# Optimization experiments

Hardware: AMD Instinct MI355X
Metric: run time of the kernel (lower is better)

Reference implementation:

```python
import jax, jax.numpy as jnp
import numpy as np

NEG = -1e30  # finite stand-in for log(0); safe for logaddexp and its gradient


def setup_inputs() -> dict:
    key = jax.random.key(0)
    k1, k2 = jax.random.split(key)
    B, T, C, U = 256, 512, 128, 128
    logits = jax.random.normal(k1, (B, T, C), dtype=jnp.float32)
    y_pred = jax.nn.softmax(logits, axis=-1)  # ctc_batch_cost expects probabilities
    y_true = jax.random.randint(k2, (B, U), 0, C - 1)  # labels exclude blank=C-1
    return {"y_true": y_true, "y_pred": y_pred}


def _ctc_batch_cost(y_true, y_pred):
    """Keras-style CTC: blank = num_classes-1, logp = log(y_pred + 1e-7),
    full input_length = T and label_length = U for every row (as in the layer).
    Returns loss of shape [B, 1]."""
    B, T, C = y_pred.shape
    U = y_true.shape[1]
    blank = C - 1
    S = 2 * U + 1  # extended label: blank-interleaved
    logp = jnp.log(y_pred + 1e-7)  # [B,T,C], keras epsilon

    # extended label sequence z = [blank, l1, blank, l2, ..., lU, blank]
    ext = jnp.full((B, S), blank, dtype=y_true.dtype).at[:, 1::2].set(y_true)

    # lp[t,b,s] = logp[b,t,ext[b,s]]
    lp = jnp.take_along_axis(logp, jnp.broadcast_to(ext[:, None, :], (B, T, S)), axis=2)
    lp = jnp.transpose(lp, (1, 0, 2))  # [T,B,S]

    # skip transition s-2 -> s allowed iff z[s] != blank and z[s] != z[s-2]
    ext_m2 = jnp.pad(ext, ((0, 0), (2, 0)), constant_values=blank)[:, :S]
    skip = (ext != blank) & (ext != ext_m2)
    skip = skip.at[:, :2].set(False)  # no s-2 predecessor for s in {0,1}

    alpha0 = jnp.full((B, S), NEG, dtype=logp.dtype)
    alpha0 = alpha0.at[:, 0].set(lp[0, :, 0]).at[:, 1].set(lp[0, :, 1])

    def step(a, lp_t):
        a1 = jnp.pad(a, ((0, 0), (1, 0)), constant_values=NEG)[:, :S]
        a2 = jnp.pad(a, ((0, 0), (2, 0)), constant_values=NEG)[:, :S]
        a2 = jnp.where(skip, a2, NEG)
        a = jnp.logaddexp(jnp.logaddexp(a, a1), a2) + lp_t
        return a, None

    aT, _ = jax.lax.scan(step, alpha0, lp[1:])
    loss = -jnp.logaddexp(aT[:, S - 1], aT[:, S - 2])
    return loss[:, None]  # [B,1], matching ctc_batch_cost output shape


def reference(y_true, y_pred):
    # The layer returns y_pred and registers the loss via add_loss; the loss is
    # the actual computation of interest, so we return it.
    return _ctc_batch_cost(y_true, y_pred)
```

## Files before the change

### kernel.cpp

```cpp
#include <hip/hip_runtime.h>

#define EPSF 1e-7f

#define DPPF0(x, ctrl) \
    __int_as_float(__builtin_amdgcn_update_dpp(0, __float_as_int(x), ctrl, 0xF, 0xF, false))

__device__ __forceinline__ float f_rcp(float x) { return __builtin_amdgcn_rcpf(x); }
__device__ __forceinline__ float wave_shr1_f(float x) { return DPPF0(x, 0x138); }

__device__ __forceinline__ float wave_max64(float x) {
    x = fmaxf(x, DPPF0(x, 0x111));
    x = fmaxf(x, DPPF0(x, 0x112));
    x = fmaxf(x, DPPF0(x, 0x114));
    x = fmaxf(x, DPPF0(x, 0x118));
    x = fmaxf(x, DPPF0(x, 0x142));
    x = fmaxf(x, DPPF0(x, 0x143));
    return __int_as_float(__builtin_amdgcn_readlane(__float_as_int(x), 63));
}

#define SB0() __builtin_amdgcn_sched_barrier(0)
#define WAITV(N) do { asm volatile("s_waitcnt vmcnt(" #N ")" ::: "memory"); SB0(); } while (0)

#define ISS(dst, voff, IMM) \
    asm volatile("global_load_dword %0, %1, %2 offset:" #IMM \
                 : "=v"(dst) : "v"(voff), "s"(pn))

#define GISSUE(X) do { \
    ISS(X##b[0], vb, 0);    ISS(X##1[0], v1, 0);    ISS(X##3[0], v3, 0); \
    ISS(X##b[1], vb, 512);  ISS(X##1[1], v1, 512);  ISS(X##3[1], v3, 512); \
    ISS(X##b[2], vb, 1024); ISS(X##1[2], v1, 1024); ISS(X##3[2], v3, 1024); \
    ISS(X##b[3], vb, 1536); ISS(X##1[3], v1, 1536); ISS(X##3[3], v3, 1536); \
    ISS(X##b[4], vb, 2048); ISS(X##1[4], v1, 2048); ISS(X##3[4], v3, 2048); \
    ISS(X##b[5], vb, 2560); ISS(X##1[5], v1, 2560); ISS(X##3[5], v3, 2560); \
    ISS(X##b[6], vb, 3072); ISS(X##1[6], v1, 3072); ISS(X##3[6], v3, 3072); \
    ISS(X##b[7], vb, 3584); ISS(X##1[7], v1, 3584); ISS(X##3[7], v3, 3584); \
    pn += 8 * 128; \
} while (0)

#define GISSUE_T7(X) do { \
    ISS(X##b[0], vb, 0);    ISS(X##1[0], v1, 0);    ISS(X##3[0], v3, 0); \
    ISS(X##b[1], vb, 512);  ISS(X##1[1], v1, 512);  ISS(X##3[1], v3, 512); \
    ISS(X##b[2], vb, 1024); ISS(X##1[2], v1, 1024); ISS(X##3[2], v3, 1024); \
    ISS(X##b[3], vb, 1536); ISS(X##1[3], v1, 1536); ISS(X##3[3], v3, 1536); \
    ISS(X##b[4], vb, 2048); ISS(X##1[4], v1, 2048); ISS(X##3[4], v3, 2048); \
    ISS(X##b[5], vb, 2560); ISS(X##1[5], v1, 2560); ISS(X##3[5], v3, 2560); \
    ISS(X##b[6], vb, 3072); ISS(X##1[6], v1, 3072); ISS(X##3[6], v3, 3072); \
} while (0)

#define PSTEP(PBE_, P1_, P3_) do { \
    const float e1 = (P1_) + EPSF; \
    const float e3 = (P3_) + EPSF; \
    const float n3 = wave_shr1_f(u3); \
    const float t1 = fmaf(m1, n3, u0 + u1); \
    const float t3 = fmaf(m3, u1, u2 + u3); \
    u4 = (u4 + u3) * (PBE_); \
    u3 = t3 * e3; \
    u2 = (u2 + u1) * (PBE_); \
    u1 = t1 * e1; \
    u0 = (u0 + n3) * (PBE_); \
} while (0)

#define SNAP(RM, LM) do { \
    float mm_ = fmaxf(fmaxf(u0, u1), fmaxf(u2, fmaxf(u3, u4))); \
    mm_ = wave_max64(mm_); \
    RM = f_rcp(mm_); \
    LM = __logf(mm_); \
} while (0)

#define APPLY(RM, LM) do { \
    u0 *= RM; u1 *= RM; u2 *= RM; u3 *= RM; u4 *= RM; \
    O += LM; \
} while (0)

#define PBE(X, k) const float pbe##k = X##b[k] + EPSF;

#define CONS8(X) do { \
    PBE(X,0) PBE(X,1) PBE(X,2) PBE(X,3) PBE(X,4) PBE(X,5) PBE(X,6) PBE(X,7) \
    PSTEP(pbe0, X##1[0], X##3[0]); \
    PSTEP(pbe1, X##1[1], X##3[1]); \
    APPLY(rmA, lmA); \
    PSTEP(pbe2, X##1[2], X##3[2]); \
    PSTEP(pbe3, X##1[3], X##3[3]); \
    SNAP(rmB, lmB); \
    PSTEP(pbe4, X##1[4], X##3[4]); \
    PSTEP(pbe5, X##1[5], X##3[5]); \
    APPLY(rmB, lmB); \
    PSTEP(pbe6, X##1[6], X##3[6]); \
    PSTEP(pbe7, X##1[7], X##3[7]); \
    SNAP(rmA, lmA); \
} while (0)

#define CONS_T7(X) do { \
    PBE(X,0) PBE(X,1) PBE(X,2) PBE(X,3) PBE(X,4) PBE(X,5) PBE(X,6) \
    PSTEP(pbe0, X##1[0], X##3[0]); \
    PSTEP(pbe1, X##1[1], X##3[1]); \
    APPLY(rmA, lmA); \
    PSTEP(pbe2, X##1[2], X##3[2]); \
    PSTEP(pbe3, X##1[3], X##3[3]); \
    SNAP(rmB, lmB); \
    PSTEP(pbe4, X##1[4], X##3[4]); \
    PSTEP(pbe5, X##1[5], X##3[5]); \
    APPLY(rmB, lmB); \
    PSTEP(pbe6, X##1[6], X##3[6]); \
} while (0)

__global__ __launch_bounds__(64, 1) void ctc_prod512(
        const int* __restrict__ y_true, const float* __restrict__ y_pred,
        float* __restrict__ out) {
    const int b    = blockIdx.x;
    const int lane = threadIdx.x;
    const float* __restrict__ yp = y_pred + (size_t)b * (512 * 128);

    const int2 lc = ((const int2*)(y_true + (size_t)b * 128))[lane];
    const int c1 = lc.x, c3 = lc.y;
    const int cp = __builtin_amdgcn_update_dpp(0, c3, 0x138, 0xF, 0xF, false);
    const float m1 = (lane > 0 && c1 != cp) ? 1.f : 0.f;
    const float m3 = (c3 != c1) ? 1.f : 0.f;

    float u0, u1, u2 = 0.f, u3 = 0.f, u4 = 0.f;
    {
        const float pvb = yp[127];
        const float pv1 = yp[c1];
        u0 = (lane == 0) ? pvb + EPSF : 0.f;
        u1 = (lane == 0) ? pv1 + EPSF : 0.f;
    }
    float O = 0.f;
    float rmA = 1.0f, lmA = 0.0f, rmB = 1.0f, lmB = 0.0f;

    const int vb = 127 * 4;
    const int v1 = c1 * 4;
    const int v3 = c3 * 4;
    const float* pn = yp + 128;

    WAITV(0);

    float Ab[8], A1[8], A3[8];
    float Bb[8], B1[8], B3[8];
    float Cb[8], C1[8], C3[8];

    GISSUE(A);
    GISSUE(B);

    for (int j = 0; j < 20; ++j) {
        WAITV(24); GISSUE(C); CONS8(A);
        WAITV(24); GISSUE(A); CONS8(B);
        WAITV(24); GISSUE(B); CONS8(C);
    }
    WAITV(24); GISSUE(C);    CONS8(A);
    WAITV(24); GISSUE_T7(A); CONS8(B);
    WAITV(21); CONS8(C);
    WAITV(0);  CONS_T7(A);

    if (lane == 63) out[b] = -(O + __logf(u3 + u4));
}

__global__ __launch_bounds__(64, 1) void ctc_scan_generic(
        const int* __restrict__ y_true, const float* __restrict__ y_pred,
        float* __restrict__ out, int T, int C, int U) {
    const int b    = blockIdx.x;
    const int lane = threadIdx.x;
    const int blank = C - 1;
    const float* __restrict__ yp = y_pred + (size_t)b * T * C;

    const int2 lc = ((const int2*)(y_true + (size_t)b * U))[lane];
    const int c1 = lc.x, c3 = lc.y;
    const int cp = __builtin_amdgcn_update_dpp(0, c3, 0x138, 0xF, 0xF, false);
    const float m1 = (lane > 0 && c1 != cp) ? 1.f : 0.f;
    const float m3 = (c3 != c1) ? 1.f : 0.f;

    float u0, u1, u2 = 0.f, u3 = 0.f, u4 = 0.f;
    u0 = (lane == 0) ? yp[blank] + EPSF : 0.f;
    u1 = (lane == 0) ? yp[c1] + EPSF : 0.f;
    float O = 0.f;
    float rmA = 1.0f, lmA = 0.0f;
    int kren = 0;

    for (int t = 1; t < T; ++t) {
        const float* row = yp + (size_t)t * C;
        const float pbe = row[blank] + EPSF;
        PSTEP(pbe, row[c1], row[c3]);
        if (++kren == 4) { SNAP(rmA, lmA); APPLY(rmA, lmA); kren = 0; }
    }
    if (lane == 63) out[b] = -(O + __logf(u3 + u4));
}

extern "C" void kernel_launch(void* const* d_in, const int* in_sizes, int n_in,
                              void* d_out, int out_size, void* d_ws, size_t ws_size,
                              hipStream_t stream) {
    const int*   y_true = (const int*)d_in[0];
    const float* y_pred = (const float*)d_in[1];
    float*       out    = (float*)d_out;

    const int B = out_size;
    const int U = in_sizes[0] / B;
    const int C = 128;
    const int T = in_sizes[1] / (B * C);

    if (T == 512 && C == 128 && U == 128) {
        ctc_prod512<<<B, 64, 0, stream>>>(y_true, y_pred, out);
    } else {
        ctc_scan_generic<<<B, 64, 0, stream>>>(y_true, y_pred, out, T, C, U);
    }
}
```

Measured before the change: 41.22 us.

## Split CTC into parallel pack pass and two-row bf16 ratio scan

Adds a pre-pass kernel that stages each batch row's probabilities through shared memory and writes label/blank probability ratios packed as two bf16 values per lane, plus the raw blank probabilities. The blank factor is pulled out of the recursion algebraically and its logs are summed in parallel up front. The scan kernel then runs two batch rows per wave, which gives more independent work to hide the serial dependency chain, and reads half as many words per step. The cost is an extra launch and a workspace round-trip, and bf16 rounding of the ratios may cost accuracy.

```diff
diff --git a/kernel.cpp b/kernel.cpp
--- a/kernel.cpp
+++ b/kernel.cpp
@@ -1,6 +1,8 @@
 #include <hip/hip_runtime.h>
 
 #define EPSF 1e-7f
+
+typedef unsigned int u32;
 
 #define DPPF0(x, ctrl) \
     __int_as_float(__builtin_amdgcn_update_dpp(0, __float_as_int(x), ctrl, 0xF, 0xF, false))
@@ -18,13 +20,223 @@
     return __int_as_float(__builtin_amdgcn_readlane(__float_as_int(x), 63));
 }
 
+__device__ __forceinline__ float wave_sum64(float x) {
+    x += DPPF0(x, 0x111);
+    x += DPPF0(x, 0x112);
+    x += DPPF0(x, 0x114);
+    x += DPPF0(x, 0x118);
+    x += DPPF0(x, 0x142);
+    x += DPPF0(x, 0x143);
+    return __int_as_float(__builtin_amdgcn_readlane(__float_as_int(x), 63));
+}
+
+__device__ __forceinline__ u32 pack_bf2(float a, float b) {
+    u32 ua = __float_as_uint(a), ub = __float_as_uint(b);
+    ua += 0x7FFFu + ((ua >> 16) & 1u);
+    ub += 0x7FFFu + ((ub >> 16) & 1u);
+    return (ua >> 16) | (ub & 0xFFFF0000u);
+}
+
+__global__ __launch_bounds__(512, 1) void ctc_pack512c(
+        const int* __restrict__ y_true, const float* __restrict__ y_pred,
+        u32* __restrict__ pk, float* __restrict__ pbf) {
+    __shared__ float stage[2][32][128];
+
+    const int b    = blockIdx.x;
+    const int tid  = threadIdx.x;
+    const int w    = tid >> 6;
+    const int lane = tid & 63;
+    const float* __restrict__ yp = y_pred + (size_t)b * (512 * 128);
+
+    const int2 lc = ((const int2*)(y_true + (size_t)b * 128))[lane];
+    const int c1 = lc.x, c3 = lc.y;
+
+    u32*   __restrict__ pkb  = pk  + (size_t)b * (512 * 64);
+    float* __restrict__ pbfb = pbf + (size_t)b * 512;
+
+    float4 r0, r1;
+    {
+        const float* src = yp;
+        r0 = *(const float4*)(src + (size_t)(tid >> 5) * 128 + ((tid & 31) << 2));
+        const int f1 = tid + 512;
+        r1 = *(const float4*)(src + (size_t)(f1 >> 5) * 128 + ((f1 & 31) << 2));
+        *(float4*)(&stage[0][tid >> 5][(tid & 31) << 2]) = r0;
+        *(float4*)(&stage[0][f1 >> 5][(f1 & 31) << 2]) = r1;
+    }
+    __syncthreads();
+
+    for (int k = 0; k < 16; ++k) {
+        if (k < 15) {
+            const float* src = yp + (size_t)(k + 1) * 32 * 128;
+            r0 = *(const float4*)(src + (size_t)(tid >> 5) * 128 + ((tid & 31) << 2));
+            const int f1 = tid + 512;
+            r1 = *(const float4*)(src + (size_t)(f1 >> 5) * 128 + ((f1 & 31) << 2));
+        }
+        {
+            const int buf = k & 1;
+            const int tb  = k * 32 + w * 4;
+#pragma unroll
+            for (int rr = 0; rr < 4; ++rr) {
+                const int r = w * 4 + rr;
+                const float p1  = stage[buf][r][c1];
+                const float p3  = stage[buf][r][c3];
+                const float pb  = stage[buf][r][127];
+                const float rpb = f_rcp(pb + EPSF);
+                pkb[(size_t)(tb + rr) * 64 + lane] =
+                    pack_bf2((p1 + EPSF) * rpb, (p3 + EPSF) * rpb);
+                if (lane == 0) pbfb[tb + rr] = pb;
+            }
+        }
+        if (k < 15) {
+            const int nb = (k + 1) & 1;
+            *(float4*)(&stage[nb][tid >> 5][(tid & 31) << 2]) = r0;
+            const int f1 = tid + 512;
+            *(float4*)(&stage[nb][f1 >> 5][(f1 & 31) << 2]) = r1;
+        }
+        __syncthreads();
+    }
+}
+
+
+#define STEPQ2(WA_, WB_) do { \
+    const u32 wa_ = (WA_), wb_ = (WB_); \
+    const float q1a = __uint_as_float(wa_ << 16); \
+    const float q3a = __uint_as_float(wa_ & 0xFFFF0000u); \
+    const float q1b = __uint_as_float(wb_ << 16); \
+    const float q3b = __uint_as_float(wb_ & 0xFFFF0000u); \
+    const float n3a = wave_shr1_f(uA3); \
+    const float n3b = wave_shr1_f(uB3); \
+    const float t1a = fmaf(m1A, n3a, uA0 + uA1); \
+    const float t1b = fmaf(m1B, n3b, uB0 + uB1); \
+    const float t3a = fmaf(m3A, uA1, uA2 + uA3); \
+    const float t3b = fmaf(m3B, uB1, uB2 + uB3); \
+    uA4 += uA3; uB4 += uB3; \
+    uA2 += uA1; uB2 += uB1; \
+    uA3 = t3a * q3a; uB3 = t3b * q3b; \
+    uA1 = t1a * q1a; uB1 = t1b * q1b; \
+    uA0 += n3a; uB0 += n3b; \
+} while (0)
+
+#define SNAPA(RM, LM) do { \
+    float mm_ = fmaxf(fmaxf(uA0, uA1), fmaxf(uA2, fmaxf(uA3, uA4))); \
+    mm_ = wave_max64(mm_); RM = f_rcp(mm_); LM = __logf(mm_); } while (0)
+#define SNAPB(RM, LM) do { \
+    float mm_ = fmaxf(fmaxf(uB0, uB1), fmaxf(uB2, fmaxf(uB3, uB4))); \
+    mm_ = wave_max64(mm_); RM = f_rcp(mm_); LM = __logf(mm_); } while (0)
+#define APPLYA(RM, LM) do { uA0*=RM; uA1*=RM; uA2*=RM; uA3*=RM; uA4*=RM; OA += LM; } while (0)
+#define APPLYB(RM, LM) do { uB0*=RM; uB1*=RM; uB2*=RM; uB3*=RM; uB4*=RM; OB += LM; } while (0)
+
+#define LDW2G(X, BASE) do { \
+    X##a0 = pkA[(size_t)((BASE)+0)*64 + lane]; X##b0 = pkB[(size_t)((BASE)+0)*64 + lane]; \
+    X##a1 = pkA[(size_t)((BASE)+1)*64 + lane]; X##b1 = pkB[(size_t)((BASE)+1)*64 + lane]; \
+    X##a2 = pkA[(size_t)((BASE)+2)*64 + lane]; X##b2 = pkB[(size_t)((BASE)+2)*64 + lane]; \
+    X##a3 = pkA[(size_t)((BASE)+3)*64 + lane]; X##b3 = pkB[(size_t)((BASE)+3)*64 + lane]; \
+    X##a4 = pkA[(size_t)((BASE)+4)*64 + lane]; X##b4 = pkB[(size_t)((BASE)+4)*64 + lane]; \
+    X##a5 = pkA[(size_t)((BASE)+5)*64 + lane]; X##b5 = pkB[(size_t)((BASE)+5)*64 + lane]; \
+    X##a6 = pkA[(size_t)((BASE)+6)*64 + lane]; X##b6 = pkB[(size_t)((BASE)+6)*64 + lane]; \
+    X##a7 = pkA[(size_t)((BASE)+7)*64 + lane]; X##b7 = pkB[(size_t)((BASE)+7)*64 + lane]; \
+} while (0)
+
+#define CONS8_2(X) do { \
+    STEPQ2(X##a0, X##b0); STEPQ2(X##a1, X##b1); \
+    APPLYA(rm1A, lm1A); APPLYB(rm1B, lm1B); \
+    STEPQ2(X##a2, X##b2); STEPQ2(X##a3, X##b3); \
+    SNAPA(rm2A, lm2A); SNAPB(rm2B, lm2B); \
+    STEPQ2(X##a4, X##b4); STEPQ2(X##a5, X##b5); \
+    APPLYA(rm2A, lm2A); APPLYB(rm2B, lm2B); \
+    STEPQ2(X##a6, X##b6); STEPQ2(X##a7, X##b7); \
+    SNAPA(rm1A, lm1A); SNAPB(rm1B, lm1B); \
+} while (0)
+
+#define CONS0_2(X) do { \
+    STEPQ2(X##a1, X##b1); STEPQ2(X##a2, X##b2); \
+    APPLYA(rm1A, lm1A); APPLYB(rm1B, lm1B); \
+    STEPQ2(X##a3, X##b3); STEPQ2(X##a4, X##b4); \
+    SNAPA(rm2A, lm2A); SNAPB(rm2B, lm2B); \
+    STEPQ2(X##a5, X##b5); STEPQ2(X##a6, X##b6); \
+    APPLYA(rm2A, lm2A); APPLYB(rm2B, lm2B); \
+    STEPQ2(X##a7, X##b7); \
+    SNAPA(rm1A, lm1A); SNAPB(rm1B, lm1B); \
+} while (0)
+
+__global__ __launch_bounds__(64, 1) void ctc_scan2r512(
+        const int* __restrict__ y_true, const float* __restrict__ y_pred,
+        const u32* __restrict__ pk, const float* __restrict__ pbf,
+        float* __restrict__ out) {
+    const int blk  = blockIdx.x;
+    const int lane = threadIdx.x;
+    const int rA = 2 * blk, rB = 2 * blk + 1;
+    const float* __restrict__ ypA = y_pred + (size_t)rA * (512 * 128);
+    const float* __restrict__ ypB = y_pred + (size_t)rB * (512 * 128);
+    const u32* __restrict__ pkA = pk + (size_t)rA * (512 * 64);
+    const u32* __restrict__ pkB = pk + (size_t)rB * (512 * 64);
+
+    const int2 lcA = ((const int2*)(y_true + (size_t)rA * 128))[lane];
+    const int2 lcB = ((const int2*)(y_true + (size_t)rB * 128))[lane];
+    const int c1A = lcA.x, c3A = lcA.y, c1B = lcB.x, c3B = lcB.y;
+
+    const int cpA = __builtin_amdgcn_update_dpp(0, c3A, 0x138, 0xF, 0xF, false);
+    const int cpB = __builtin_amdgcn_update_dpp(0, c3B, 0x138, 0xF, 0xF, false);
+    const float m1A = (lane > 0 && c1A != cpA) ? 1.f : 0.f;
+    const float m3A = (c3A != c1A) ? 1.f : 0.f;
+    const float m1B = (lane > 0 && c1B != cpB) ? 1.f : 0.f;
+    const float m3B = (c3B != c1B) ? 1.f : 0.f;
+
+    float blsA = 0.f, blsB = 0.f;
+    {
+        const float* pA = pbf + (size_t)rA * 512 + lane * 8;
+        const float* pB = pbf + (size_t)rB * 512 + lane * 8;
+        const float4 a0 = *(const float4*)(pA);
+        const float4 a1 = *(const float4*)(pA + 4);
+        const float4 b0 = *(const float4*)(pB);
+        const float4 b1 = *(const float4*)(pB + 4);
+        float sa = __logf(a0.y + EPSF) + __logf(a0.z + EPSF) + __logf(a0.w + EPSF)
+                 + __logf(a1.x + EPSF) + __logf(a1.y + EPSF) + __logf(a1.z + EPSF)
+                 + __logf(a1.w + EPSF);
+        float sb = __logf(b0.y + EPSF) + __logf(b0.z + EPSF) + __logf(b0.w + EPSF)
+                 + __logf(b1.x + EPSF) + __logf(b1.y + EPSF) + __logf(b1.z + EPSF)
+                 + __logf(b1.w + EPSF);
+        if (lane > 0) { sa += __logf(a0.x + EPSF); sb += __logf(b0.x + EPSF); }
+        blsA = wave_sum64(sa);
+        blsB = wave_sum64(sb);
+    }
+
+    float uA0 = (lane == 0) ? ypA[127] + EPSF : 0.f;
+    float uA1 = (lane == 0) ? ypA[c1A] + EPSF : 0.f;
+    float uA2 = 0.f, uA3 = 0.f, uA4 = 0.f;
+    float uB0 = (lane == 0) ? ypB[127] + EPSF : 0.f;
+    float uB1 = (lane == 0) ? ypB[c1B] + EPSF : 0.f;
+    float uB2 = 0.f, uB3 = 0.f, uB4 = 0.f;
+    float OA = 0.f, OB = 0.f;
+    float rm1A = 1.f, lm1A = 0.f, rm2A = 1.f, lm2A = 0.f;
+    float rm1B = 1.f, lm1B = 0.f, rm2B = 1.f, lm2B = 0.f;
+
+    u32 Pa0, Pa1, Pa2, Pa3, Pa4, Pa5, Pa6, Pa7;
+    u32 Pb0, Pb1, Pb2, Pb3, Pb4, Pb5, Pb6, Pb7;
+    u32 Qa0, Qa1, Qa2, Qa3, Qa4, Qa5, Qa6, Qa7;
+    u32 Qb0, Qb1, Qb2, Qb3, Qb4, Qb5, Qb6, Qb7;
+
+    LDW2G(P, 0);
+    LDW2G(Q, 8);
+    CONS0_2(P);
+
+    for (int j = 0; j < 31; ++j) {
+        LDW2G(P, 16 * j + 16); CONS8_2(Q);
+        LDW2G(Q, 16 * j + 24); CONS8_2(P);
+    }
+    CONS8_2(Q);
+
+    if (lane == 63) {
+        out[rA] = -(OA + blsA + __logf(uA3 + uA4));
+        out[rB] = -(OB + blsB + __logf(uB3 + uB4));
+    }
+}
+
 #define SB0() __builtin_amdgcn_sched_barrier(0)
 #define WAITV(N) do { asm volatile("s_waitcnt vmcnt(" #N ")" ::: "memory"); SB0(); } while (0)
-
 #define ISS(dst, voff, IMM) \
     asm volatile("global_load_dword %0, %1, %2 offset:" #IMM \
                  : "=v"(dst) : "v"(voff), "s"(pn))
-
 #define GISSUE(X) do { \
     ISS(X##b[0], vb, 0);    ISS(X##1[0], v1, 0);    ISS(X##3[0], v3, 0); \
     ISS(X##b[1], vb, 512);  ISS(X##1[1], v1, 512);  ISS(X##3[1], v3, 512); \
@@ -36,7 +248,6 @@
     ISS(X##b[7], vb, 3584); ISS(X##1[7], v1, 3584); ISS(X##3[7], v3, 3584); \
     pn += 8 * 128; \
 } while (0)
-
 #define GISSUE_T7(X) do { \
     ISS(X##b[0], vb, 0);    ISS(X##1[0], v1, 0);    ISS(X##3[0], v3, 0); \
     ISS(X##b[1], vb, 512);  ISS(X##1[1], v1, 512);  ISS(X##3[1], v3, 512); \
@@ -46,7 +257,6 @@
     ISS(X##b[5], vb, 2560); ISS(X##1[5], v1, 2560); ISS(X##3[5], v3, 2560); \
     ISS(X##b[6], vb, 3072); ISS(X##1[6], v1, 3072); ISS(X##3[6], v3, 3072); \
 } while (0)
-
 #define PSTEP(PBE_, P1_, P3_) do { \
     const float e1 = (P1_) + EPSF; \
     const float e3 = (P3_) + EPSF; \
@@ -59,23 +269,19 @@
     u1 = t1 * e1; \
     u0 = (u0 + n3) * (PBE_); \
 } while (0)
-
 #define SNAP(RM, LM) do { \
     float mm_ = fmaxf(fmaxf(u0, u1), fmaxf(u2, fmaxf(u3, u4))); \
     mm_ = wave_max64(mm_); \
     RM = f_rcp(mm_); \
     LM = __logf(mm_); \
 } while (0)
-
 #define APPLY(RM, LM) do { \
     u0 *= RM; u1 *= RM; u2 *= RM; u3 *= RM; u4 *= RM; \
     O += LM; \
 } while (0)
-
-#define PBE(X, k) const float pbe##k = X##b[k] + EPSF;
-
+#define PBED(X, k) const float pbe##k = X##b[k] + EPSF;
 #define CONS8(X) do { \
-    PBE(X,0) PBE(X,1) PBE(X,2) PBE(X,3) PBE(X,4) PBE(X,5) PBE(X,6) PBE(X,7) \
+    PBED(X,0) PBED(X,1) PBED(X,2) PBED(X,3) PBED(X,4) PBED(X,5) PBED(X,6) PBED(X,7) \
     PSTEP(pbe0, X##1[0], X##3[0]); \
     PSTEP(pbe1, X##1[1], X##3[1]); \
     APPLY(rmA, lmA); \
@@ -89,9 +295,8 @@
     PSTEP(pbe7, X##1[7], X##3[7]); \
     SNAP(rmA, lmA); \
 } while (0)
-
 #define CONS_T7(X) do { \
-    PBE(X,0) PBE(X,1) PBE(X,2) PBE(X,3) PBE(X,4) PBE(X,5) PBE(X,6) \
+    PBED(X,0) PBED(X,1) PBED(X,2) PBED(X,3) PBED(X,4) PBED(X,5) PBED(X,6) \
     PSTEP(pbe0, X##1[0], X##3[0]); \
     PSTEP(pbe1, X##1[1], X##3[1]); \
     APPLY(rmA, lmA); \
@@ -168,9 +373,9 @@
     const float m1 = (lane > 0 && c1 != cp) ? 1.f : 0.f;
     const float m3 = (c3 != c1) ? 1.f : 0.f;
 
-    float u0, u1, u2 = 0.f, u3 = 0.f, u4 = 0.f;
-    u0 = (lane == 0) ? yp[blank] + EPSF : 0.f;
-    u1 = (lane == 0) ? yp[c1] + EPSF : 0.f;
+    float u0 = (lane == 0) ? yp[blank] + EPSF : 0.f;
+    float u1 = (lane == 0) ? yp[c1] + EPSF : 0.f;
+    float u2 = 0.f, u3 = 0.f, u4 = 0.f;
     float O = 0.f;
     float rmA = 1.0f, lmA = 0.0f;
     int kren = 0;
@@ -178,8 +383,23 @@
     for (int t = 1; t < T; ++t) {
         const float* row = yp + (size_t)t * C;
         const float pbe = row[blank] + EPSF;
-        PSTEP(pbe, row[c1], row[c3]);
-        if (++kren == 4) { SNAP(rmA, lmA); APPLY(rmA, lmA); kren = 0; }
+        const float rpb = f_rcp(pbe);
+        const float q1  = (row[c1] + EPSF) * rpb;
+        const float q3  = (row[c3] + EPSF) * rpb;
+        const float n3  = wave_shr1_f(u3);
+        const float t1  = fmaf(m1, n3, u0 + u1);
+        const float t3  = fmaf(m3, u1, u2 + u3);
+        u4 = u4 + u3;
+        u3 = t3 * q3;
+        u2 = u2 + u1;
+        u1 = t1 * q1;
+        u0 = u0 + n3;
+        O += __logf(pbe);
+        if (++kren == 4) {
+            SNAP(rmA, lmA);
+            APPLY(rmA, lmA);
+            kren = 0;
+        }
     }
     if (lane == 63) out[b] = -(O + __logf(u3 + u4));
 }
@@ -196,8 +416,17 @@
     const int C = 128;
     const int T = in_sizes[1] / (B * C);
 
-    if (T == 512 && C == 128 && U == 128) {
-        ctc_prod512<<<B, 64, 0, stream>>>(y_true, y_pred, out);
+    if (T == 512 && C == 128 && U == 128 && (B & 1) == 0) {
+        const size_t pk_bytes = (size_t)B * 512 * 64 * 4;
+        const size_t need     = pk_bytes + (size_t)B * 512 * 4;
+        if (ws_size >= need) {
+            u32*   pkw = (u32*)d_ws;
+            float* pbf = (float*)((char*)d_ws + pk_bytes);
+            ctc_pack512c<<<B, 512, 0, stream>>>(y_true, y_pred, pkw, pbf);
+            ctc_scan2r512<<<B / 2, 64, 0, stream>>>(y_true, y_pred, pkw, pbf, out);
+        } else {
+            ctc_prod512<<<B, 64, 0, stream>>>(y_true, y_pred, out);
+        }
     } else {
         ctc_scan_generic<<<B, 64, 0, stream>>>(y_true, y_pred, out, T, C, U);
     }
```

Result: slower. 83.24 us (+102.0%).
